# Kernel optimization log

Hardware: AMD Instinct MI355X
Metric: run time of the kernel (lower is better)

## Reference

```python
import jax, jax.numpy as jnp
import numpy as np

NODE_DIM = 3
EMBED = 16


def _gcn_mean_conv(x, W, b, src, dst, ew, N):
    """PyG GCNConv with aggr='mean': self-loops (weight 1), symmetric norm, mean agg, bias."""
    xw = x @ W  # [N, out]
    loop = jnp.arange(N, dtype=src.dtype)
    src2 = jnp.concatenate([src, loop])
    dst2 = jnp.concatenate([dst, loop])
    ew2 = jnp.concatenate([ew, jnp.ones((N,), x.dtype)])
    deg = jax.ops.segment_sum(ew2, dst2, num_segments=N)
    dinv = jnp.where(deg > 0, jax.lax.rsqrt(jnp.maximum(deg, 1e-12)), 0.0)
    norm = dinv[src2] * ew2 * dinv[dst2]  # [E+N]
    msg = norm[:, None] * xw[src2]  # [E+N, out]
    s = jax.ops.segment_sum(msg, dst2, num_segments=N)
    cnt = jax.ops.segment_sum(jnp.ones_like(norm), dst2, num_segments=N)
    return s / cnt[:, None] + b


def setup_inputs() -> dict:
    key = jax.random.key(0)
    ks = jax.random.split(key, 12)
    N, E, G, A = 500000, 8000000, 10000, 50
    pos = jax.random.normal(ks[0], (N, NODE_DIM), jnp.float32)
    sigmas = jax.random.uniform(ks[1], (G, A), jnp.float32, 0.1, 1.0)
    edge_index = jax.random.randint(ks[2], (2, E), 0, N, jnp.int64)

    def lin(k, fi, fo):
        k1, k2 = jax.random.split(k)
        lim = 1.0 / np.sqrt(fi)
        return (jax.random.uniform(k1, (fi, fo), jnp.float32, -lim, lim),
                jax.random.uniform(k2, (fo,), jnp.float32, -lim, lim))

    W_init, b_init = lin(ks[3], NODE_DIM, EMBED)
    W_g1, b_g1 = lin(ks[4], EMBED, EMBED)
    W_g2, b_g2 = lin(ks[5], EMBED, EMBED)
    W_p1, b_p1 = lin(ks[6], EMBED, EMBED)
    W_p2, b_p2 = lin(ks[7], EMBED, NODE_DIM)
    return {"pos": pos, "sigmas": sigmas, "edge_index": edge_index, "num_graphs": G,
            "W_init": W_init, "b_init": b_init, "W_g1": W_g1, "b_g1": b_g1,
            "W_g2": W_g2, "b_g2": b_g2, "W_p1": W_p1, "b_p1": b_p1,
            "W_p2": W_p2, "b_p2": b_p2}


def reference(pos, sigmas, edge_index, num_graphs, W_init, b_init, W_g1, b_g1,
              W_g2, b_g2, W_p1, b_p1, W_p2, b_p2):
    N = pos.shape[0]
    src, dst = edge_index[0], edge_index[1]
    edge_weight = jnp.linalg.norm(pos[src] - pos[dst], axis=1)  # [E]
    sp = jax.nn.softplus
    x = sp(pos @ W_init + b_init)
    x = sp(_gcn_mean_conv(x, W_g1, b_g1, src, dst, edge_weight, N))
    x = sp(_gcn_mean_conv(x, W_g2, b_g2, src, dst, edge_weight, N))
    y = sp(x @ W_p1 + b_p1)
    scores = (y @ W_p2 + b_p2).reshape(num_graphs, -1, NODE_DIM)
    scores = scores / sigmas[:, :, None]
    return scores.reshape(-1, NODE_DIM)
```

## Files before the change

kernel.cpp:

```cpp
#include <hip/hip_runtime.h>
#include <hip/hip_bf16.h>
#include <hip/hip_fp16.h>
#include <math.h>

#define ND 3
#define EM 16
#define BQ 512
#define BQ_SH 9
#define MAXB 1024
#define CHK 8192
#define COLS 12288
#define P_SH 23

__device__ __forceinline__ float sp(float x) {
    return fmaxf(x, 0.0f) + log1pf(expf(-fabsf(x)));
}

__global__ __launch_bounds__(1024) void bucket_zero(int* __restrict__ bcnt)
{
    bcnt[threadIdx.x] = 0;
}

__global__ __launch_bounds__(256) void bucket_count(
    const int* __restrict__ ei, int* __restrict__ bcnt, int E, int NB)
{
    __shared__ int h[MAXB];
    int t = threadIdx.x;
    for (int i = t; i < MAXB; i += 256) h[i] = 0;
    __syncthreads();
    const int* dp = ei + (size_t)E;
    for (int e = blockIdx.x * 256 + t; e < E; e += gridDim.x * 256)
        atomicAdd(&h[((unsigned)dp[e]) >> BQ_SH], 1);
    __syncthreads();
    for (int i = t; i < NB; i += 256) {
        int v = h[i];
        if (v) atomicAdd(&bcnt[i], v);
    }
}

__global__ __launch_bounds__(1024) void bucket_scan(
    const int* __restrict__ bcnt, int* __restrict__ gbase,
    int* __restrict__ gcur, int NB)
{
    __shared__ int sd[1024];
    int t = threadIdx.x;
    int v = (t < NB) ? bcnt[t] : 0;
    sd[t] = v;
    __syncthreads();
    for (int off = 1; off < 1024; off <<= 1) {
        int add = (t >= off) ? sd[t - off] : 0;
        __syncthreads();
        sd[t] += add;
        __syncthreads();
    }
    if (t < NB) { int ex = sd[t] - v; gbase[t] = ex; gcur[t] = ex; }
}

__global__ __launch_bounds__(256) void edge_bin(
    const int* __restrict__ ei, int* __restrict__ gcur,
    unsigned int* __restrict__ pairs, int E)
{
    __shared__ int lcnt[MAXB];
    __shared__ int lbase[MAXB];
    __shared__ int sbase[MAXB];
    __shared__ unsigned int stage[CHK];
    __shared__ unsigned short bid[CHK];
    __shared__ int sd[256];
    int t = threadIdx.x;
    int c0 = blockIdx.x * CHK;
    int cntT = min(CHK, E - c0);
    for (int i = t; i < MAXB; i += 256) lcnt[i] = 0;
    __syncthreads();
    const int* dp = ei + (size_t)E;
    int dreg[32];
#pragma unroll
    for (int it = 0; it < 32; it++) {
        int e = c0 + it * 256 + t;
        dreg[it] = (e < E) ? dp[e] : 0;
        if (e < E) atomicAdd(&lcnt[((unsigned)dreg[it]) >> BQ_SH], 1);
    }
    __syncthreads();
    int b4 = t * 4;
    int h0 = lcnt[b4], h1 = lcnt[b4 + 1], h2 = lcnt[b4 + 2], h3 = lcnt[b4 + 3];
    int s4 = h0 + h1 + h2 + h3;
    sd[t] = s4;
    __syncthreads();
    for (int off = 1; off < 256; off <<= 1) {
        int add = (t >= off) ? sd[t - off] : 0;
        __syncthreads();
        sd[t] += add;
        __syncthreads();
    }
    int ex = sd[t] - s4;
    lbase[b4]     = ex;
    lbase[b4 + 1] = ex + h0;
    lbase[b4 + 2] = ex + h0 + h1;
    lbase[b4 + 3] = ex + h0 + h1 + h2;
    sbase[b4]     = h0 ? atomicAdd(&gcur[b4], h0)     : 0;
    sbase[b4 + 1] = h1 ? atomicAdd(&gcur[b4 + 1], h1) : 0;
    sbase[b4 + 2] = h2 ? atomicAdd(&gcur[b4 + 2], h2) : 0;
    sbase[b4 + 3] = h3 ? atomicAdd(&gcur[b4 + 3], h3) : 0;
    lcnt[b4] = 0; lcnt[b4 + 1] = 0; lcnt[b4 + 2] = 0; lcnt[b4 + 3] = 0;
    __syncthreads();
#pragma unroll
    for (int it = 0; it < 32; it++) {
        int e = c0 + it * 256 + t;
        if (e < E) {
            int d = dreg[it];
            unsigned b = ((unsigned)d) >> BQ_SH;
            int s = ei[e];
            int pos = lbase[b] + atomicAdd(&lcnt[b], 1);
            stage[pos] = ((unsigned)(d & (BQ - 1)) << P_SH) | (unsigned)s;
            bid[pos] = (unsigned short)b;
        }
    }
    __syncthreads();
    for (int i = t; i < cntT; i += 256) {
        unsigned b = bid[i];
        pairs[sbase[b] + (i - lbase[b])] = stage[i];
    }
}

__global__ __launch_bounds__(256) void bucket_csr(
    const unsigned int* __restrict__ pairs, const int* __restrict__ gbase,
    const int* __restrict__ bcnt, const float* __restrict__ pos,
    int* __restrict__ rowptr, int2* __restrict__ cw,
    float* __restrict__ dinv, int N, int NB)
{
    __shared__ int ncnt[BQ];
    __shared__ int ncur[BQ];
    __shared__ float wsum[BQ];
    __shared__ int sd[256];
    __shared__ unsigned int stg[COLS];
    __shared__ float posS[BQ * 3];
    int b = blockIdx.x;
    int t = threadIdx.x;
    int lo = b << BQ_SH;
    int hi = min(lo + BQ, N);
    int nloc = hi - lo;
    int r0 = gbase[b];
    int cntE = bcnt[b];
    for (int i = t; i < 3 * nloc; i += 256) posS[i] = pos[(size_t)lo * 3 + i];
    ncnt[2 * t] = 0;
    ncnt[2 * t + 1] = 0;
    wsum[2 * t] = 0.0f;
    wsum[2 * t + 1] = 0.0f;
    __syncthreads();
    for (int i = t; i < cntE; i += 256)
        atomicAdd(&ncnt[pairs[r0 + i] >> P_SH], 1);
    __syncthreads();
    int a0 = ncnt[2 * t], a1 = ncnt[2 * t + 1];
    int s2 = a0 + a1;
    sd[t] = s2;
    __syncthreads();
    for (int off = 1; off < 256; off <<= 1) {
        int add = (t >= off) ? sd[t - off] : 0;
        __syncthreads();
        sd[t] += add;
        __syncthreads();
    }
    int ex = sd[t] - s2;
    ncur[2 * t] = ex;
    ncur[2 * t + 1] = ex + a0;
    if (lo + 2 * t < hi)     rowptr[lo + 2 * t]     = r0 + ex;
    if (lo + 2 * t + 1 < hi) rowptr[lo + 2 * t + 1] = r0 + ex + a0;
    if (b == NB - 1 && t == 0) rowptr[N] = r0 + cntE;
    __syncthreads();
    bool fit = (cntE <= COLS);
    if (fit) {
        for (int i = t; i < cntE; i += 256) {
            unsigned p = pairs[r0 + i];
            int slot = atomicAdd(&ncur[p >> P_SH], 1);
            stg[slot] = p;
        }
        __syncthreads();
        for (int i = t; i < cntE; i += 256) {
            unsigned p = stg[i];
            int ldst = (int)(p >> P_SH);
            int src = (int)(p & ((1u << P_SH) - 1));
            float dx = posS[ldst * 3 + 0] - pos[(size_t)src * 3 + 0];
            float dy = posS[ldst * 3 + 1] - pos[(size_t)src * 3 + 1];
            float dz = posS[ldst * 3 + 2] - pos[(size_t)src * 3 + 2];
            float d = sqrtf(fmaf(dx, dx, fmaf(dy, dy, dz * dz)));
            cw[r0 + i] = make_int2(src, __float_as_int(d));
            atomicAdd(&wsum[ldst], d);
        }
    } else {
        for (int i = t; i < cntE; i += 256) {
            unsigned p = pairs[r0 + i];
            int ldst = (int)(p >> P_SH);
            int src = (int)(p & ((1u << P_SH) - 1));
            int slot = atomicAdd(&ncur[ldst], 1);
            float dx = posS[ldst * 3 + 0] - pos[(size_t)src * 3 + 0];
            float dy = posS[ldst * 3 + 1] - pos[(size_t)src * 3 + 1];
            float dz = posS[ldst * 3 + 2] - pos[(size_t)src * 3 + 2];
            float d = sqrtf(fmaf(dx, dx, fmaf(dy, dy, dz * dz)));
            cw[r0 + slot] = make_int2(src, __float_as_int(d));
            atomicAdd(&wsum[ldst], d);
        }
    }
    __syncthreads();
    for (int l = t; l < nloc; l += 256)
        dinv[lo + l] = rsqrtf(1.0f + wsum[l]);
}

__global__ __launch_bounds__(256) void node_init(
    const float* __restrict__ pos,
    const float* __restrict__ W_init, const float* __restrict__ b_init,
    const float* __restrict__ W_g1, const float* __restrict__ dinv,
    __half2* __restrict__ zh1, int N)
{
    __shared__ float sWi[ND * EM];
    __shared__ float sbi[EM];
    __shared__ float sW1[EM * EM];
    int t = threadIdx.x;
    if (t < ND * EM) sWi[t] = W_init[t];
    if (t < EM)      sbi[t] = b_init[t];
    sW1[t] = W_g1[t];
    __syncthreads();

    int n = blockIdx.x * 256 + t;
    if (n >= N) return;

    float p0 = pos[3 * (size_t)n + 0];
    float p1 = pos[3 * (size_t)n + 1];
    float p2 = pos[3 * (size_t)n + 2];

    float x0[EM];
#pragma unroll
    for (int j = 0; j < EM; j++) {
        float h = fmaf(p0, sWi[0 * EM + j],
                  fmaf(p1, sWi[1 * EM + j],
                  fmaf(p2, sWi[2 * EM + j], sbi[j])));
        x0[j] = sp(h);
    }
    float di = dinv[n];
    __half2* zo = zh1 + (size_t)n * 8;
#pragma unroll
    for (int k = 0; k < 8; k++) {
        float ax = 0.0f, ay = 0.0f;
#pragma unroll
        for (int j = 0; j < EM; j++) {
            ax = fmaf(x0[j], sW1[j * EM + 2 * k], ax);
            ay = fmaf(x0[j], sW1[j * EM + 2 * k + 1], ay);
        }
        zo[k] = __float22half2_rn(make_float2(ax * di, ay * di));
    }
}

__global__ __launch_bounds__(256) void gather_conv(
    const int* __restrict__ rowptr, const int2* __restrict__ cw,
    const float* __restrict__ dinv, const __half2* __restrict__ zin,
    const float* __restrict__ bconv, const float* __restrict__ W,
    __half2* __restrict__ zout, float* __restrict__ fout, int N, int mulW)
{
    __shared__ float sW[EM * EM];
    __shared__ float lx[32][EM + 1];
    int t = threadIdx.x;
    sW[t] = W[t];
    int g = t >> 3, c = t & 7;
    int n = blockIdx.x * 32 + g;

    float xx = 0.0f, xy = 0.0f;
    float di = 1.0f;
    if (n < N) {
        int start = rowptr[n], end = rowptr[n + 1];
        di = dinv[n];
        float2 zv = __half22float2(zin[(size_t)n * 8 + c]);
        float a0x = zv.x, a0y = zv.y;
        float a1x = 0.f, a1y = 0.f, a2x = 0.f, a2y = 0.f, a3x = 0.f, a3y = 0.f;
        int j = start;
        for (; j + 3 < end; j += 4) {
            int2 e0 = cw[j], e1 = cw[j + 1], e2 = cw[j + 2], e3 = cw[j + 3];
            float2 z0 = __half22float2(zin[(size_t)e0.x * 8 + c]);
            float2 z1 = __half22float2(zin[(size_t)e1.x * 8 + c]);
            float2 z2 = __half22float2(zin[(size_t)e2.x * 8 + c]);
            float2 z3 = __half22float2(zin[(size_t)e3.x * 8 + c]);
            float w0 = __int_as_float(e0.y), w1 = __int_as_float(e1.y);
            float w2 = __int_as_float(e2.y), w3 = __int_as_float(e3.y);
            a0x = fmaf(w0, z0.x, a0x); a0y = fmaf(w0, z0.y, a0y);
            a1x = fmaf(w1, z1.x, a1x); a1y = fmaf(w1, z1.y, a1y);
            a2x = fmaf(w2, z2.x, a2x); a2y = fmaf(w2, z2.y, a2y);
            a3x = fmaf(w3, z3.x, a3x); a3y = fmaf(w3, z3.y, a3y);
        }
        for (; j < end; j++) {
            int2 e = cw[j];
            float2 zr = __half22float2(zin[(size_t)e.x * 8 + c]);
            float wv = __int_as_float(e.y);
            a0x = fmaf(wv, zr.x, a0x); a0y = fmaf(wv, zr.y, a0y);
        }
        float accx = (a0x + a1x) + (a2x + a3x);
        float accy = (a0y + a1y) + (a2y + a3y);
        float rc = 1.0f / (float)(end - start + 1);
        xx = sp(fmaf(accx * di, rc, bconv[2 * c]));
        xy = sp(fmaf(accy * di, rc, bconv[2 * c + 1]));
    }
    __syncthreads();
    lx[g][2 * c]     = xx;
    lx[g][2 * c + 1] = xy;
    __syncthreads();
    if (n < N) {
        if (mulW) {
            float ax = 0.0f, ay = 0.0f;
#pragma unroll
            for (int j = 0; j < EM; j++) {
                float lj = lx[g][j];
                ax = fmaf(lj, sW[j * EM + 2 * c], ax);
                ay = fmaf(lj, sW[j * EM + 2 * c + 1], ay);
            }
            zout[(size_t)n * 8 + c] =
                __float22half2_rn(make_float2(ax * di, ay * di));
        } else {
            float* xo = fout + (size_t)n * EM + 2 * c;
            xo[0] = xx;
            xo[1] = xy;
        }
    }
}

__global__ __launch_bounds__(256) void node_out(
    const float* __restrict__ W_p1, const float* __restrict__ b_p1,
    const float* __restrict__ W_p2, const float* __restrict__ b_p2,
    const float* __restrict__ sig, const float* __restrict__ x2arr,
    float* __restrict__ out, int N)
{
    __shared__ float sP1[EM * EM];
    __shared__ float sbp1[EM];
    __shared__ float sP2[EM * ND];
    __shared__ float sbp2[ND];
    int t = threadIdx.x;
    sP1[t] = W_p1[t];
    if (t < EM)      sbp1[t] = b_p1[t];
    if (t < EM * ND) sP2[t] = W_p2[t];
    if (t < ND)      sbp2[t] = b_p2[t];
    __syncthreads();

    int n = blockIdx.x * 256 + t;
    if (n >= N) return;

    const float4* xp = (const float4*)(x2arr + (size_t)n * EM);
    float x2[EM];
#pragma unroll
    for (int q = 0; q < 4; q++) {
        float4 xv = xp[q];
        x2[4*q+0] = xv.x; x2[4*q+1] = xv.y; x2[4*q+2] = xv.z; x2[4*q+3] = xv.w;
    }
    float y[EM];
#pragma unroll
    for (int k = 0; k < EM; k++) {
        float a = sbp1[k];
#pragma unroll
        for (int j = 0; j < EM; j++) a = fmaf(x2[j], sP1[j * EM + k], a);
        y[k] = sp(a);
    }
    float rs = 1.0f / sig[n];
#pragma unroll
    for (int ch = 0; ch < ND; ch++) {
        float a = sbp2[ch];
#pragma unroll
        for (int j = 0; j < EM; j++) a = fmaf(y[j], sP2[j * ND + ch], a);
        out[(size_t)n * ND + ch] = a * rs;
    }
}

extern "C" void kernel_launch(void* const* d_in, const int* in_sizes, int n_in,
                              void* d_out, int out_size, void* d_ws, size_t ws_size,
                              hipStream_t stream) {
    const float* pos    = (const float*)d_in[0];
    const float* sig    = (const float*)d_in[1];
    const int*   ei     = (const int*)d_in[2];
    const float* W_init = (const float*)d_in[4];
    const float* b_init = (const float*)d_in[5];
    const float* W_g1   = (const float*)d_in[6];
    const float* b_g1   = (const float*)d_in[7];
    const float* W_g2   = (const float*)d_in[8];
    const float* b_g2   = (const float*)d_in[9];
    const float* W_p1   = (const float*)d_in[10];
    const float* b_p1   = (const float*)d_in[11];
    const float* W_p2   = (const float*)d_in[12];
    const float* b_p2   = (const float*)d_in[13];
    float* out = (float*)d_out;

    int N = in_sizes[0] / ND;
    int E = in_sizes[2] / 2;
    size_t Ns = (size_t)N, Es = (size_t)E;
    int NB = (N + BQ - 1) >> BQ_SH;

    int* rowptr = (int*)d_ws;
    size_t cwoff = (Ns + 2) & ~(size_t)1;
    int2* cw    = (int2*)((int*)d_ws + cwoff);
    int* bcnt   = (int*)(cw + Es);
    int* gbase  = bcnt + 1024;
    int* gcur   = gbase + 1024;
    size_t off  = cwoff + 2 * Es + 3 * 1024;
    off = (off + 3) & ~(size_t)3;
    float* dinv = (float*)d_ws + off;
    size_t offA = off + Ns;
    offA = (offA + 3) & ~(size_t)3;
    float* xf32 = (float*)d_ws + offA;
    __half2* zh1 = (__half2*)(xf32 + Ns * EM);
    __half2* zh2 = (__half2*)((float*)(xf32 + Ns * EM) + Ns * 8);
    unsigned int* pairs = (unsigned int*)xf32;

    int nbN = (N + 255) / 256;
    int nbG2 = (N + 31) / 32;
    int nbBin = (E + CHK - 1) / CHK;

    bucket_zero<<<1, 1024, 0, stream>>>(bcnt);
    bucket_count<<<1024, 256, 0, stream>>>(ei, bcnt, E, NB);
    bucket_scan<<<1, 1024, 0, stream>>>(bcnt, gbase, gcur, NB);
    edge_bin<<<nbBin, 256, 0, stream>>>(ei, gcur, pairs, E);
    bucket_csr<<<NB, 256, 0, stream>>>(pairs, gbase, bcnt, pos, rowptr, cw, dinv, N, NB);
    node_init<<<nbN, 256, 0, stream>>>(pos, W_init, b_init, W_g1, dinv, zh1, N);
    gather_conv<<<nbG2, 256, 0, stream>>>(rowptr, cw, dinv, zh1, b_g1, W_g2, zh2, (float*)0, N, 1);
    gather_conv<<<nbG2, 256, 0, stream>>>(rowptr, cw, dinv, zh2, b_g2, W_g2, (__half2*)0, xf32, N, 0);
    node_out<<<nbN, 256, 0, stream>>>(W_p1, b_p1, W_p2, b_p2, sig, xf32, out, N);
}
```

Before: 784.5 us.

## Fuse node init into CSR build and replace per-node gather with shared-memory bucket scatter

The CSR build now also computes the per-node initial embedding and the reciprocal in-degree, so the separate node_init kernel is gone. The per-node rowptr gather is replaced by a per-bucket kernel. It walks the bucket's edges, which are now grouped into eight source-index ranges to improve gather locality, and accumulates messages with float atomics into a 512-node shared-memory tile. The second convolution also fuses the output MLP and the sigma division, which removes the fp32 intermediate buffer and one launch. In exchange it relies on many shared-memory atomics, and the final layer reads a row after lanes of the same wave write it without a barrier.

```diff
diff --git a/kernel.cpp b/kernel.cpp
--- a/kernel.cpp
+++ b/kernel.cpp
@@ -1,5 +1,4 @@
 #include <hip/hip_runtime.h>
-#include <hip/hip_bf16.h>
 #include <hip/hip_fp16.h>
 #include <math.h>
 
@@ -11,6 +10,9 @@
 #define CHK 8192
 #define COLS 12288
 #define P_SH 23
+#define PMASK ((1u << P_SH) - 1)
+#define RSH 16
+#define NRANGE 8
 
 __device__ __forceinline__ float sp(float x) {
     return fmaxf(x, 0.0f) + log1pf(expf(-fabsf(x)));
@@ -121,245 +123,225 @@
     }
 }
 
-__global__ __launch_bounds__(256) void bucket_csr(
+__global__ __launch_bounds__(256) void bucket_csr_init(
     const unsigned int* __restrict__ pairs, const int* __restrict__ gbase,
     const int* __restrict__ bcnt, const float* __restrict__ pos,
-    int* __restrict__ rowptr, int2* __restrict__ cw,
-    float* __restrict__ dinv, int N, int NB)
-{
-    __shared__ int ncnt[BQ];
-    __shared__ int ncur[BQ];
+    const float* __restrict__ W_init, const float* __restrict__ b_init,
+    const float* __restrict__ W_g1,
+    int* __restrict__ rb8, int2* __restrict__ cw2,
+    float* __restrict__ dinv, float* __restrict__ rcarr,
+    __half2* __restrict__ zh1, int N, int NB)
+{
+    __shared__ float posS[BQ * 3];
+    __shared__ unsigned int stg[COLS];
     __shared__ float wsum[BQ];
-    __shared__ int sd[256];
-    __shared__ unsigned int stg[COLS];
-    __shared__ float posS[BQ * 3];
-    int b = blockIdx.x;
-    int t = threadIdx.x;
+    __shared__ int dcnt[BQ];
+    __shared__ int r8cnt[NRANGE];
+    __shared__ int r8cur[NRANGE];
+    __shared__ float sWi[ND * EM];
+    __shared__ float sbi[EM];
+    __shared__ float sW1[EM * EM];
+    int b = blockIdx.x, t = threadIdx.x;
     int lo = b << BQ_SH;
     int hi = min(lo + BQ, N);
     int nloc = hi - lo;
     int r0 = gbase[b];
     int cntE = bcnt[b];
+    if (t < ND * EM) sWi[t] = W_init[t];
+    if (t < EM)      sbi[t] = b_init[t];
+    sW1[t] = W_g1[t];
     for (int i = t; i < 3 * nloc; i += 256) posS[i] = pos[(size_t)lo * 3 + i];
-    ncnt[2 * t] = 0;
-    ncnt[2 * t + 1] = 0;
-    wsum[2 * t] = 0.0f;
-    wsum[2 * t + 1] = 0.0f;
-    __syncthreads();
-    for (int i = t; i < cntE; i += 256)
-        atomicAdd(&ncnt[pairs[r0 + i] >> P_SH], 1);
-    __syncthreads();
-    int a0 = ncnt[2 * t], a1 = ncnt[2 * t + 1];
-    int s2 = a0 + a1;
-    sd[t] = s2;
-    __syncthreads();
-    for (int off = 1; off < 256; off <<= 1) {
-        int add = (t >= off) ? sd[t - off] : 0;
-        __syncthreads();
-        sd[t] += add;
-        __syncthreads();
-    }
-    int ex = sd[t] - s2;
-    ncur[2 * t] = ex;
-    ncur[2 * t + 1] = ex + a0;
-    if (lo + 2 * t < hi)     rowptr[lo + 2 * t]     = r0 + ex;
-    if (lo + 2 * t + 1 < hi) rowptr[lo + 2 * t + 1] = r0 + ex + a0;
-    if (b == NB - 1 && t == 0) rowptr[N] = r0 + cntE;
+    wsum[2 * t] = 0.0f; wsum[2 * t + 1] = 0.0f;
+    dcnt[2 * t] = 0;    dcnt[2 * t + 1] = 0;
+    if (t < NRANGE) r8cnt[t] = 0;
+    __syncthreads();
+    for (int i = t; i < cntE; i += 256) {
+        unsigned p = pairs[r0 + i];
+        atomicAdd(&r8cnt[(p & PMASK) >> RSH], 1);
+        atomicAdd(&dcnt[p >> P_SH], 1);
+    }
+    __syncthreads();
+    if (t == 0) {
+        int run = 0;
+        for (int r = 0; r < NRANGE; r++) {
+            int v = r8cnt[r];
+            r8cur[r] = run;
+            rb8[b * NRANGE + r] = r0 + run;
+            run += v;
+        }
+    }
     __syncthreads();
     bool fit = (cntE <= COLS);
     if (fit) {
         for (int i = t; i < cntE; i += 256) {
             unsigned p = pairs[r0 + i];
-            int slot = atomicAdd(&ncur[p >> P_SH], 1);
+            int slot = atomicAdd(&r8cur[(p & PMASK) >> RSH], 1);
             stg[slot] = p;
         }
         __syncthreads();
         for (int i = t; i < cntE; i += 256) {
             unsigned p = stg[i];
             int ldst = (int)(p >> P_SH);
-            int src = (int)(p & ((1u << P_SH) - 1));
+            int src  = (int)(p & PMASK);
             float dx = posS[ldst * 3 + 0] - pos[(size_t)src * 3 + 0];
             float dy = posS[ldst * 3 + 1] - pos[(size_t)src * 3 + 1];
             float dz = posS[ldst * 3 + 2] - pos[(size_t)src * 3 + 2];
-            float d = sqrtf(fmaf(dx, dx, fmaf(dy, dy, dz * dz)));
-            cw[r0 + i] = make_int2(src, __float_as_int(d));
-            atomicAdd(&wsum[ldst], d);
+            float w = sqrtf(fmaf(dx, dx, fmaf(dy, dy, dz * dz)));
+            cw2[r0 + i] = make_int2((int)p, __float_as_int(w));
+            atomicAdd(&wsum[ldst], w);
         }
     } else {
         for (int i = t; i < cntE; i += 256) {
             unsigned p = pairs[r0 + i];
             int ldst = (int)(p >> P_SH);
-            int src = (int)(p & ((1u << P_SH) - 1));
-            int slot = atomicAdd(&ncur[ldst], 1);
+            int src  = (int)(p & PMASK);
+            int slot = atomicAdd(&r8cur[(p & PMASK) >> RSH], 1);
             float dx = posS[ldst * 3 + 0] - pos[(size_t)src * 3 + 0];
             float dy = posS[ldst * 3 + 1] - pos[(size_t)src * 3 + 1];
             float dz = posS[ldst * 3 + 2] - pos[(size_t)src * 3 + 2];
-            float d = sqrtf(fmaf(dx, dx, fmaf(dy, dy, dz * dz)));
-            cw[r0 + slot] = make_int2(src, __float_as_int(d));
-            atomicAdd(&wsum[ldst], d);
-        }
-    }
-    __syncthreads();
-    for (int l = t; l < nloc; l += 256)
-        dinv[lo + l] = rsqrtf(1.0f + wsum[l]);
-}
-
-__global__ __launch_bounds__(256) void node_init(
-    const float* __restrict__ pos,
-    const float* __restrict__ W_init, const float* __restrict__ b_init,
-    const float* __restrict__ W_g1, const float* __restrict__ dinv,
-    __half2* __restrict__ zh1, int N)
-{
-    __shared__ float sWi[ND * EM];
-    __shared__ float sbi[EM];
-    __shared__ float sW1[EM * EM];
-    int t = threadIdx.x;
-    if (t < ND * EM) sWi[t] = W_init[t];
-    if (t < EM)      sbi[t] = b_init[t];
-    sW1[t] = W_g1[t];
-    __syncthreads();
-
-    int n = blockIdx.x * 256 + t;
-    if (n >= N) return;
-
-    float p0 = pos[3 * (size_t)n + 0];
-    float p1 = pos[3 * (size_t)n + 1];
-    float p2 = pos[3 * (size_t)n + 2];
-
-    float x0[EM];
-#pragma unroll
-    for (int j = 0; j < EM; j++) {
-        float h = fmaf(p0, sWi[0 * EM + j],
-                  fmaf(p1, sWi[1 * EM + j],
-                  fmaf(p2, sWi[2 * EM + j], sbi[j])));
-        x0[j] = sp(h);
-    }
-    float di = dinv[n];
-    __half2* zo = zh1 + (size_t)n * 8;
-#pragma unroll
-    for (int k = 0; k < 8; k++) {
-        float ax = 0.0f, ay = 0.0f;
+            float w = sqrtf(fmaf(dx, dx, fmaf(dy, dy, dz * dz)));
+            cw2[r0 + slot] = make_int2((int)p, __float_as_int(w));
+            atomicAdd(&wsum[ldst], w);
+        }
+    }
+    __syncthreads();
+    for (int l = t; l < nloc; l += 256) {
+        int n = lo + l;
+        float di = rsqrtf(1.0f + wsum[l]);
+        dinv[n] = di;
+        rcarr[n] = 1.0f / (float)(dcnt[l] + 1);
+        float p0 = posS[l * 3 + 0];
+        float p1 = posS[l * 3 + 1];
+        float p2 = posS[l * 3 + 2];
+        float x0[EM];
 #pragma unroll
         for (int j = 0; j < EM; j++) {
-            ax = fmaf(x0[j], sW1[j * EM + 2 * k], ax);
-            ay = fmaf(x0[j], sW1[j * EM + 2 * k + 1], ay);
-        }
-        zo[k] = __float22half2_rn(make_float2(ax * di, ay * di));
-    }
-}
-
-__global__ __launch_bounds__(256) void gather_conv(
-    const int* __restrict__ rowptr, const int2* __restrict__ cw,
-    const float* __restrict__ dinv, const __half2* __restrict__ zin,
-    const float* __restrict__ bconv, const float* __restrict__ W,
-    __half2* __restrict__ zout, float* __restrict__ fout, int N, int mulW)
-{
+            float h = fmaf(p0, sWi[0 * EM + j],
+                      fmaf(p1, sWi[1 * EM + j],
+                      fmaf(p2, sWi[2 * EM + j], sbi[j])));
+            x0[j] = sp(h);
+        }
+        __half2* zo = zh1 + (size_t)n * 8;
+#pragma unroll
+        for (int k = 0; k < 8; k++) {
+            float ax = 0.0f, ay = 0.0f;
+#pragma unroll
+            for (int j = 0; j < EM; j++) {
+                ax = fmaf(x0[j], sW1[j * EM + 2 * k], ax);
+                ay = fmaf(x0[j], sW1[j * EM + 2 * k + 1], ay);
+            }
+            zo[k] = __float22half2_rn(make_float2(ax * di, ay * di));
+        }
+    }
+}
+
+__global__ __launch_bounds__(256) void conv_p(
+    const int* __restrict__ rb8, const int* __restrict__ gbase,
+    const int* __restrict__ bcnt, const int2* __restrict__ cw2,
+    const float* __restrict__ dinv, const float* __restrict__ rcarr,
+    const __half2* __restrict__ zin, const float* __restrict__ bconv,
+    const float* __restrict__ W,
+    const float* __restrict__ P1, const float* __restrict__ b1,
+    const float* __restrict__ P2, const float* __restrict__ b2,
+    const float* __restrict__ sig,
+    __half2* __restrict__ zout, float* __restrict__ out,
+    int N, int mode)
+{
+    __shared__ float acc[BQ][EM + 2];
     __shared__ float sW[EM * EM];
-    __shared__ float lx[32][EM + 1];
-    int t = threadIdx.x;
-    sW[t] = W[t];
+    __shared__ float sb[EM];
+    __shared__ float sP1[EM * EM];
+    __shared__ float sb1[EM];
+    __shared__ float sP2[EM * ND];
+    __shared__ float sb2[ND];
+    __shared__ int rbL[NRANGE + 1];
+    int b = blockIdx.x, t = threadIdx.x;
+    int lo = b << BQ_SH;
+    if (mode == 1) {
+        sW[t] = W[t];
+    } else {
+        sP1[t] = P1[t];
+        if (t < EM)      sb1[t] = b1[t];
+        if (t < EM * ND) sP2[t] = P2[t];
+        if (t < ND)      sb2[t] = b2[t];
+    }
+    if (t < EM) sb[t] = bconv[t];
+    if (t < NRANGE) rbL[t] = rb8[b * NRANGE + t];
+    if (t == NRANGE) rbL[NRANGE] = gbase[b] + bcnt[b];
+    float* ap = &acc[0][0];
+    for (int i = t; i < BQ * (EM + 2); i += 256) ap[i] = 0.0f;
+    __syncthreads();
+
     int g = t >> 3, c = t & 7;
-    int n = blockIdx.x * 32 + g;
-
-    float xx = 0.0f, xy = 0.0f;
-    float di = 1.0f;
-    if (n < N) {
-        int start = rowptr[n], end = rowptr[n + 1];
-        di = dinv[n];
-        float2 zv = __half22float2(zin[(size_t)n * 8 + c]);
-        float a0x = zv.x, a0y = zv.y;
-        float a1x = 0.f, a1y = 0.f, a2x = 0.f, a2y = 0.f, a3x = 0.f, a3y = 0.f;
-        int j = start;
-        for (; j + 3 < end; j += 4) {
-            int2 e0 = cw[j], e1 = cw[j + 1], e2 = cw[j + 2], e3 = cw[j + 3];
-            float2 z0 = __half22float2(zin[(size_t)e0.x * 8 + c]);
-            float2 z1 = __half22float2(zin[(size_t)e1.x * 8 + c]);
-            float2 z2 = __half22float2(zin[(size_t)e2.x * 8 + c]);
-            float2 z3 = __half22float2(zin[(size_t)e3.x * 8 + c]);
-            float w0 = __int_as_float(e0.y), w1 = __int_as_float(e1.y);
-            float w2 = __int_as_float(e2.y), w3 = __int_as_float(e3.y);
-            a0x = fmaf(w0, z0.x, a0x); a0y = fmaf(w0, z0.y, a0y);
-            a1x = fmaf(w1, z1.x, a1x); a1y = fmaf(w1, z1.y, a1y);
-            a2x = fmaf(w2, z2.x, a2x); a2y = fmaf(w2, z2.y, a2y);
-            a3x = fmaf(w3, z3.x, a3x); a3y = fmaf(w3, z3.y, a3y);
-        }
-        for (; j < end; j++) {
-            int2 e = cw[j];
-            float2 zr = __half22float2(zin[(size_t)e.x * 8 + c]);
-            float wv = __int_as_float(e.y);
-            a0x = fmaf(wv, zr.x, a0x); a0y = fmaf(wv, zr.y, a0y);
-        }
-        float accx = (a0x + a1x) + (a2x + a3x);
-        float accy = (a0y + a1y) + (a2y + a3y);
-        float rc = 1.0f / (float)(end - start + 1);
-        xx = sp(fmaf(accx * di, rc, bconv[2 * c]));
-        xy = sp(fmaf(accy * di, rc, bconv[2 * c + 1]));
-    }
-    __syncthreads();
-    lx[g][2 * c]     = xx;
-    lx[g][2 * c + 1] = xy;
-    __syncthreads();
-    if (n < N) {
-        if (mulW) {
+    for (int r = 0; r < NRANGE; r++) {
+        int ee = rbL[r + 1];
+        for (int e0 = rbL[r] + g * 8; e0 < ee; e0 += 32 * 8) {
+            int2 cwv = (e0 + c < ee) ? cw2[e0 + c] : make_int2(0, 0);
+            unsigned pk[8]; float wv[8];
+#pragma unroll
+            for (int k = 0; k < 8; k++) {
+                pk[k] = (unsigned)__shfl(cwv.x, k, 8);
+                wv[k] = __int_as_float(__shfl(cwv.y, k, 8));
+            }
+            __half2 zz[8];
+#pragma unroll
+            for (int k = 0; k < 8; k++)
+                zz[k] = zin[(size_t)(pk[k] & PMASK) * 8 + c];
+#pragma unroll
+            for (int k = 0; k < 8; k++) {
+                float2 z = __half22float2(zz[k]);
+                int nl = (int)(pk[k] >> P_SH);
+                atomicAdd(&acc[nl][2 * c],     wv[k] * z.x);
+                atomicAdd(&acc[nl][2 * c + 1], wv[k] * z.y);
+            }
+        }
+    }
+    __syncthreads();
+    for (int j = 0; j < 16; j++) {
+        int nl = j * 32 + g;
+        int n = lo + nl;
+        if (n < N) {
+            float ax = acc[nl][2 * c], ay = acc[nl][2 * c + 1];
+            float2 s = __half22float2(zin[(size_t)n * 8 + c]);
+            float di = dinv[n], rc = rcarr[n];
+            acc[nl][2 * c]     = sp(fmaf((ax + s.x) * di, rc, sb[2 * c]));
+            acc[nl][2 * c + 1] = sp(fmaf((ay + s.y) * di, rc, sb[2 * c + 1]));
+        }
+    }
+    __syncthreads();
+    for (int j = 0; j < 16; j++) {
+        int nl = j * 32 + g;
+        int n = lo + nl;
+        if (n >= N) continue;
+        if (mode == 1) {
+            float di = dinv[n];
             float ax = 0.0f, ay = 0.0f;
 #pragma unroll
-            for (int j = 0; j < EM; j++) {
-                float lj = lx[g][j];
-                ax = fmaf(lj, sW[j * EM + 2 * c], ax);
-                ay = fmaf(lj, sW[j * EM + 2 * c + 1], ay);
+            for (int jj = 0; jj < EM; jj++) {
+                float v = acc[nl][jj];
+                ax = fmaf(v, sW[jj * EM + 2 * c], ax);
+                ay = fmaf(v, sW[jj * EM + 2 * c + 1], ay);
             }
             zout[(size_t)n * 8 + c] =
                 __float22half2_rn(make_float2(ax * di, ay * di));
         } else {
-            float* xo = fout + (size_t)n * EM + 2 * c;
-            xo[0] = xx;
-            xo[1] = xy;
-        }
-    }
-}
-
-__global__ __launch_bounds__(256) void node_out(
-    const float* __restrict__ W_p1, const float* __restrict__ b_p1,
-    const float* __restrict__ W_p2, const float* __restrict__ b_p2,
-    const float* __restrict__ sig, const float* __restrict__ x2arr,
-    float* __restrict__ out, int N)
-{
-    __shared__ float sP1[EM * EM];
-    __shared__ float sbp1[EM];
-    __shared__ float sP2[EM * ND];
-    __shared__ float sbp2[ND];
-    int t = threadIdx.x;
-    sP1[t] = W_p1[t];
-    if (t < EM)      sbp1[t] = b_p1[t];
-    if (t < EM * ND) sP2[t] = W_p2[t];
-    if (t < ND)      sbp2[t] = b_p2[t];
-    __syncthreads();
-
-    int n = blockIdx.x * 256 + t;
-    if (n >= N) return;
-
-    const float4* xp = (const float4*)(x2arr + (size_t)n * EM);
-    float x2[EM];
-#pragma unroll
-    for (int q = 0; q < 4; q++) {
-        float4 xv = xp[q];
-        x2[4*q+0] = xv.x; x2[4*q+1] = xv.y; x2[4*q+2] = xv.z; x2[4*q+3] = xv.w;
-    }
-    float y[EM];
-#pragma unroll
-    for (int k = 0; k < EM; k++) {
-        float a = sbp1[k];
-#pragma unroll
-        for (int j = 0; j < EM; j++) a = fmaf(x2[j], sP1[j * EM + k], a);
-        y[k] = sp(a);
-    }
-    float rs = 1.0f / sig[n];
-#pragma unroll
-    for (int ch = 0; ch < ND; ch++) {
-        float a = sbp2[ch];
-#pragma unroll
-        for (int j = 0; j < EM; j++) a = fmaf(y[j], sP2[j * ND + ch], a);
-        out[(size_t)n * ND + ch] = a * rs;
+            float ax = sb1[2 * c], ay = sb1[2 * c + 1];
+#pragma unroll
+            for (int jj = 0; jj < EM; jj++) {
+                float v = acc[nl][jj];
+                ax = fmaf(v, sP1[jj * EM + 2 * c], ax);
+                ay = fmaf(v, sP1[jj * EM + 2 * c + 1], ay);
+            }
+            acc[nl][2 * c]     = sp(ax);
+            acc[nl][2 * c + 1] = sp(ay);
+            if (c < ND) {
+                float o = sb2[c];
+#pragma unroll
+                for (int jj = 0; jj < EM; jj++)
+                    o = fmaf(acc[nl][jj], sP2[jj * ND + c], o);
+                out[(size_t)n * ND + c] = o / sig[n];
+            }
+        }
     }
 }
 
@@ -386,33 +368,29 @@
     size_t Ns = (size_t)N, Es = (size_t)E;
     int NB = (N + BQ - 1) >> BQ_SH;
 
-    int* rowptr = (int*)d_ws;
-    size_t cwoff = (Ns + 2) & ~(size_t)1;
-    int2* cw    = (int2*)((int*)d_ws + cwoff);
-    int* bcnt   = (int*)(cw + Es);
-    int* gbase  = bcnt + 1024;
-    int* gcur   = gbase + 1024;
-    size_t off  = cwoff + 2 * Es + 3 * 1024;
-    off = (off + 3) & ~(size_t)3;
-    float* dinv = (float*)d_ws + off;
-    size_t offA = off + Ns;
-    offA = (offA + 3) & ~(size_t)3;
-    float* xf32 = (float*)d_ws + offA;
-    __half2* zh1 = (__half2*)(xf32 + Ns * EM);
-    __half2* zh2 = (__half2*)((float*)(xf32 + Ns * EM) + Ns * 8);
-    unsigned int* pairs = (unsigned int*)xf32;
-
-    int nbN = (N + 255) / 256;
-    int nbG2 = (N + 31) / 32;
+    int* bcnt  = (int*)d_ws;
+    int* gbase = bcnt + 1024;
+    int* gcur  = gbase + 1024;
+    int* rb8   = gcur + 1024;
+    float* dinv  = (float*)(rb8 + 8 * MAXB);
+    float* rcarr = dinv + Ns;
+    size_t off = 3 * 1024 + 8 * MAXB + 2 * Ns;
+    off = (off + 1) & ~(size_t)1;
+    int2* cw2 = (int2*)((int*)d_ws + off);
+    unsigned int* pairs = (unsigned int*)(cw2 + Es);
+    __half2* zh2 = (__half2*)pairs;
+    __half2* zh1 = (__half2*)(pairs + Es);
+
     int nbBin = (E + CHK - 1) / CHK;
 
     bucket_zero<<<1, 1024, 0, stream>>>(bcnt);
     bucket_count<<<1024, 256, 0, stream>>>(ei, bcnt, E, NB);
     bucket_scan<<<1, 1024, 0, stream>>>(bcnt, gbase, gcur, NB);
     edge_bin<<<nbBin, 256, 0, stream>>>(ei, gcur, pairs, E);
-    bucket_csr<<<NB, 256, 0, stream>>>(pairs, gbase, bcnt, pos, rowptr, cw, dinv, N, NB);
-    node_init<<<nbN, 256, 0, stream>>>(pos, W_init, b_init, W_g1, dinv, zh1, N);
-    gather_conv<<<nbG2, 256, 0, stream>>>(rowptr, cw, dinv, zh1, b_g1, W_g2, zh2, (float*)0, N, 1);
-    gather_conv<<<nbG2, 256, 0, stream>>>(rowptr, cw, dinv, zh2, b_g2, W_g2, (__half2*)0, xf32, N, 0);
-    node_out<<<nbN, 256, 0, stream>>>(W_p1, b_p1, W_p2, b_p2, sig, xf32, out, N);
-}
+    bucket_csr_init<<<NB, 256, 0, stream>>>(pairs, gbase, bcnt, pos,
+        W_init, b_init, W_g1, rb8, cw2, dinv, rcarr, zh1, N, NB);
+    conv_p<<<NB, 256, 0, stream>>>(rb8, gbase, bcnt, cw2, dinv, rcarr,
+        zh1, b_g1, W_g2, W_p1, b_p1, W_p2, b_p2, sig, zh2, out, N, 1);
+    conv_p<<<NB, 256, 0, stream>>>(rb8, gbase, bcnt, cw2, dinv, rcarr,
+        zh2, b_g2, W_g2, W_p1, b_p1, W_p2, b_p2, sig, zh2, out, N, 2);
+}
```

Result: slower. 1.909 ms (+143.4%).

## Fuse node init into CSR build and output MLP into second conv

Applied to the files above, without the earlier changes.

Folds the per-node init (initial linear plus softplus, W_g1 projection, dinv scaling) into the tail of the bucket CSR kernel, reusing positions already staged in shared memory. It also folds the output MLP and sigma division into the second gather_conv through a mode flag. This removes two kernel launches and the fp32 N×16 intermediate write and re-read. The workspace is repacked so zh2 reuses the pairs buffer once the CSR is built. The mode-2 path overwrites the lx tile while other lanes of the same node group are still reading it, with no barrier, so it relies on wavefront lockstep for correctness.

```diff
diff --git a/kernel.cpp b/kernel.cpp
--- a/kernel.cpp
+++ b/kernel.cpp
@@ -1,5 +1,4 @@
 #include <hip/hip_runtime.h>
-#include <hip/hip_bf16.h>
 #include <hip/hip_fp16.h>
 #include <math.h>
 
@@ -11,6 +10,7 @@
 #define CHK 8192
 #define COLS 12288
 #define P_SH 23
+#define PMASK ((1u << P_SH) - 1)
 
 __device__ __forceinline__ float sp(float x) {
     return fmaxf(x, 0.0f) + log1pf(expf(-fabsf(x)));
@@ -121,11 +121,13 @@
     }
 }
 
-__global__ __launch_bounds__(256) void bucket_csr(
+__global__ __launch_bounds__(256) void bucket_csr_init(
     const unsigned int* __restrict__ pairs, const int* __restrict__ gbase,
     const int* __restrict__ bcnt, const float* __restrict__ pos,
+    const float* __restrict__ W_init, const float* __restrict__ b_init,
+    const float* __restrict__ W_g1,
     int* __restrict__ rowptr, int2* __restrict__ cw,
-    float* __restrict__ dinv, int N, int NB)
+    float* __restrict__ dinv, __half2* __restrict__ zh1, int N, int NB)
 {
     __shared__ int ncnt[BQ];
     __shared__ int ncur[BQ];
@@ -133,6 +135,9 @@
     __shared__ int sd[256];
     __shared__ unsigned int stg[COLS];
     __shared__ float posS[BQ * 3];
+    __shared__ float sWi[ND * EM];
+    __shared__ float sbi[EM];
+    __shared__ float sW1[EM * EM];
     int b = blockIdx.x;
     int t = threadIdx.x;
     int lo = b << BQ_SH;
@@ -140,6 +145,9 @@
     int nloc = hi - lo;
     int r0 = gbase[b];
     int cntE = bcnt[b];
+    if (t < ND * EM) sWi[t] = W_init[t];
+    if (t < EM)      sbi[t] = b_init[t];
+    sW1[t] = W_g1[t];
     for (int i = t; i < 3 * nloc; i += 256) posS[i] = pos[(size_t)lo * 3 + i];
     ncnt[2 * t] = 0;
     ncnt[2 * t + 1] = 0;
@@ -177,7 +185,7 @@
         for (int i = t; i < cntE; i += 256) {
             unsigned p = stg[i];
             int ldst = (int)(p >> P_SH);
-            int src = (int)(p & ((1u << P_SH) - 1));
+            int src = (int)(p & PMASK);
             float dx = posS[ldst * 3 + 0] - pos[(size_t)src * 3 + 0];
             float dy = posS[ldst * 3 + 1] - pos[(size_t)src * 3 + 1];
             float dz = posS[ldst * 3 + 2] - pos[(size_t)src * 3 + 2];
@@ -189,7 +197,7 @@
         for (int i = t; i < cntE; i += 256) {
             unsigned p = pairs[r0 + i];
             int ldst = (int)(p >> P_SH);
-            int src = (int)(p & ((1u << P_SH) - 1));
+            int src = (int)(p & PMASK);
             int slot = atomicAdd(&ncur[ldst], 1);
             float dx = posS[ldst * 3 + 0] - pos[(size_t)src * 3 + 0];
             float dy = posS[ldst * 3 + 1] - pos[(size_t)src * 3 + 1];
@@ -200,51 +208,32 @@
         }
     }
     __syncthreads();
-    for (int l = t; l < nloc; l += 256)
-        dinv[lo + l] = rsqrtf(1.0f + wsum[l]);
-}
-
-__global__ __launch_bounds__(256) void node_init(
-    const float* __restrict__ pos,
-    const float* __restrict__ W_init, const float* __restrict__ b_init,
-    const float* __restrict__ W_g1, const float* __restrict__ dinv,
-    __half2* __restrict__ zh1, int N)
-{
-    __shared__ float sWi[ND * EM];
-    __shared__ float sbi[EM];
-    __shared__ float sW1[EM * EM];
-    int t = threadIdx.x;
-    if (t < ND * EM) sWi[t] = W_init[t];
-    if (t < EM)      sbi[t] = b_init[t];
-    sW1[t] = W_g1[t];
-    __syncthreads();
-
-    int n = blockIdx.x * 256 + t;
-    if (n >= N) return;
-
-    float p0 = pos[3 * (size_t)n + 0];
-    float p1 = pos[3 * (size_t)n + 1];
-    float p2 = pos[3 * (size_t)n + 2];
-
-    float x0[EM];
-#pragma unroll
-    for (int j = 0; j < EM; j++) {
-        float h = fmaf(p0, sWi[0 * EM + j],
-                  fmaf(p1, sWi[1 * EM + j],
-                  fmaf(p2, sWi[2 * EM + j], sbi[j])));
-        x0[j] = sp(h);
-    }
-    float di = dinv[n];
-    __half2* zo = zh1 + (size_t)n * 8;
-#pragma unroll
-    for (int k = 0; k < 8; k++) {
-        float ax = 0.0f, ay = 0.0f;
+    for (int l = t; l < nloc; l += 256) {
+        int n = lo + l;
+        float di = rsqrtf(1.0f + wsum[l]);
+        dinv[n] = di;
+        float p0 = posS[l * 3 + 0];
+        float p1 = posS[l * 3 + 1];
+        float p2 = posS[l * 3 + 2];
+        float x0[EM];
 #pragma unroll
         for (int j = 0; j < EM; j++) {
-            ax = fmaf(x0[j], sW1[j * EM + 2 * k], ax);
-            ay = fmaf(x0[j], sW1[j * EM + 2 * k + 1], ay);
-        }
-        zo[k] = __float22half2_rn(make_float2(ax * di, ay * di));
+            float h = fmaf(p0, sWi[0 * EM + j],
+                      fmaf(p1, sWi[1 * EM + j],
+                      fmaf(p2, sWi[2 * EM + j], sbi[j])));
+            x0[j] = sp(h);
+        }
+        __half2* zo = zh1 + (size_t)n * 8;
+#pragma unroll
+        for (int k = 0; k < 8; k++) {
+            float ax = 0.0f, ay = 0.0f;
+#pragma unroll
+            for (int j = 0; j < EM; j++) {
+                ax = fmaf(x0[j], sW1[j * EM + 2 * k], ax);
+                ay = fmaf(x0[j], sW1[j * EM + 2 * k + 1], ay);
+            }
+            zo[k] = __float22half2_rn(make_float2(ax * di, ay * di));
+        }
     }
 }
 
@@ -252,12 +241,25 @@
     const int* __restrict__ rowptr, const int2* __restrict__ cw,
     const float* __restrict__ dinv, const __half2* __restrict__ zin,
     const float* __restrict__ bconv, const float* __restrict__ W,
-    __half2* __restrict__ zout, float* __restrict__ fout, int N, int mulW)
+    const float* __restrict__ P1, const float* __restrict__ b1,
+    const float* __restrict__ P2, const float* __restrict__ b2,
+    const float* __restrict__ sig,
+    __half2* __restrict__ zout, float* __restrict__ out, int N, int mode)
 {
     __shared__ float sW[EM * EM];
+    __shared__ float sP2[EM * ND];
+    __shared__ float sb1[EM];
+    __shared__ float sb2[ND];
     __shared__ float lx[32][EM + 1];
     int t = threadIdx.x;
-    sW[t] = W[t];
+    if (mode == 1) {
+        sW[t] = W[t];
+    } else {
+        sW[t] = P1[t];
+        if (t < EM)      sb1[t] = b1[t];
+        if (t < EM * ND) sP2[t] = P2[t];
+        if (t < ND)      sb2[t] = b2[t];
+    }
     int g = t >> 3, c = t & 7;
     int n = blockIdx.x * 32 + g;
 
@@ -300,7 +302,7 @@
     lx[g][2 * c + 1] = xy;
     __syncthreads();
     if (n < N) {
-        if (mulW) {
+        if (mode == 1) {
             float ax = 0.0f, ay = 0.0f;
 #pragma unroll
             for (int j = 0; j < EM; j++) {
@@ -311,55 +313,23 @@
             zout[(size_t)n * 8 + c] =
                 __float22half2_rn(make_float2(ax * di, ay * di));
         } else {
-            float* xo = fout + (size_t)n * EM + 2 * c;
-            xo[0] = xx;
-            xo[1] = xy;
-        }
-    }
-}
-
-__global__ __launch_bounds__(256) void node_out(
-    const float* __restrict__ W_p1, const float* __restrict__ b_p1,
-    const float* __restrict__ W_p2, const float* __restrict__ b_p2,
-    const float* __restrict__ sig, const float* __restrict__ x2arr,
-    float* __restrict__ out, int N)
-{
-    __shared__ float sP1[EM * EM];
-    __shared__ float sbp1[EM];
-    __shared__ float sP2[EM * ND];
-    __shared__ float sbp2[ND];
-    int t = threadIdx.x;
-    sP1[t] = W_p1[t];
-    if (t < EM)      sbp1[t] = b_p1[t];
-    if (t < EM * ND) sP2[t] = W_p2[t];
-    if (t < ND)      sbp2[t] = b_p2[t];
-    __syncthreads();
-
-    int n = blockIdx.x * 256 + t;
-    if (n >= N) return;
-
-    const float4* xp = (const float4*)(x2arr + (size_t)n * EM);
-    float x2[EM];
-#pragma unroll
-    for (int q = 0; q < 4; q++) {
-        float4 xv = xp[q];
-        x2[4*q+0] = xv.x; x2[4*q+1] = xv.y; x2[4*q+2] = xv.z; x2[4*q+3] = xv.w;
-    }
-    float y[EM];
-#pragma unroll
-    for (int k = 0; k < EM; k++) {
-        float a = sbp1[k];
-#pragma unroll
-        for (int j = 0; j < EM; j++) a = fmaf(x2[j], sP1[j * EM + k], a);
-        y[k] = sp(a);
-    }
-    float rs = 1.0f / sig[n];
-#pragma unroll
-    for (int ch = 0; ch < ND; ch++) {
-        float a = sbp2[ch];
-#pragma unroll
-        for (int j = 0; j < EM; j++) a = fmaf(y[j], sP2[j * ND + ch], a);
-        out[(size_t)n * ND + ch] = a * rs;
+            float ax = sb1[2 * c], ay = sb1[2 * c + 1];
+#pragma unroll
+            for (int j = 0; j < EM; j++) {
+                float lj = lx[g][j];
+                ax = fmaf(lj, sW[j * EM + 2 * c], ax);
+                ay = fmaf(lj, sW[j * EM + 2 * c + 1], ay);
+            }
+            lx[g][2 * c]     = sp(ax);
+            lx[g][2 * c + 1] = sp(ay);
+            if (c < ND) {
+                float o = sb2[c];
+#pragma unroll
+                for (int j = 0; j < EM; j++)
+                    o = fmaf(lx[g][j], sP2[j * ND + c], o);
+                out[(size_t)n * ND + c] = o / sig[n];
+            }
+        }
     }
 }
 
@@ -387,22 +357,17 @@
     int NB = (N + BQ - 1) >> BQ_SH;
 
     int* rowptr = (int*)d_ws;
-    size_t cwoff = (Ns + 2) & ~(size_t)1;
-    int2* cw    = (int2*)((int*)d_ws + cwoff);
-    int* bcnt   = (int*)(cw + Es);
+    int* bcnt   = rowptr + (Ns + 1);
     int* gbase  = bcnt + 1024;
     int* gcur   = gbase + 1024;
-    size_t off  = cwoff + 2 * Es + 3 * 1024;
-    off = (off + 3) & ~(size_t)3;
-    float* dinv = (float*)d_ws + off;
-    size_t offA = off + Ns;
-    offA = (offA + 3) & ~(size_t)3;
-    float* xf32 = (float*)d_ws + offA;
-    __half2* zh1 = (__half2*)(xf32 + Ns * EM);
-    __half2* zh2 = (__half2*)((float*)(xf32 + Ns * EM) + Ns * 8);
-    unsigned int* pairs = (unsigned int*)xf32;
-
-    int nbN = (N + 255) / 256;
+    float* dinv = (float*)(gcur + 1024);
+    size_t off = (Ns + 1) + 3 * 1024 + Ns;
+    off = (off + 1) & ~(size_t)1;
+    int2* cw = (int2*)((int*)d_ws + off);
+    unsigned int* pairs = (unsigned int*)(cw + Es);
+    __half2* zh2 = (__half2*)pairs;
+    __half2* zh1 = (__half2*)(pairs + Es);
+
     int nbG2 = (N + 31) / 32;
     int nbBin = (E + CHK - 1) / CHK;
 
@@ -410,9 +375,10 @@
     bucket_count<<<1024, 256, 0, stream>>>(ei, bcnt, E, NB);
     bucket_scan<<<1, 1024, 0, stream>>>(bcnt, gbase, gcur, NB);
     edge_bin<<<nbBin, 256, 0, stream>>>(ei, gcur, pairs, E);
-    bucket_csr<<<NB, 256, 0, stream>>>(pairs, gbase, bcnt, pos, rowptr, cw, dinv, N, NB);
-    node_init<<<nbN, 256, 0, stream>>>(pos, W_init, b_init, W_g1, dinv, zh1, N);
-    gather_conv<<<nbG2, 256, 0, stream>>>(rowptr, cw, dinv, zh1, b_g1, W_g2, zh2, (float*)0, N, 1);
-    gather_conv<<<nbG2, 256, 0, stream>>>(rowptr, cw, dinv, zh2, b_g2, W_g2, (__half2*)0, xf32, N, 0);
-    node_out<<<nbN, 256, 0, stream>>>(W_p1, b_p1, W_p2, b_p2, sig, xf32, out, N);
-}
+    bucket_csr_init<<<NB, 256, 0, stream>>>(pairs, gbase, bcnt, pos,
+        W_init, b_init, W_g1, rowptr, cw, dinv, zh1, N, NB);
+    gather_conv<<<nbG2, 256, 0, stream>>>(rowptr, cw, dinv, zh1, b_g1, W_g2,
+        W_p1, b_p1, W_p2, b_p2, sig, zh2, out, N, 1);
+    gather_conv<<<nbG2, 256, 0, stream>>>(rowptr, cw, dinv, zh2, b_g2, W_g2,
+        W_p1, b_p1, W_p2, b_p2, sig, zh2, out, N, 2);
+}
```

After: 786.3 us. About the same (+0.2%).
